# Performance work log

Measured on AMD Instinct MI355X. Metric: run time of the kernel, lower is better.

The kernel has to match this reference:

```python
import jax, jax.numpy as jnp
import numpy as np

B, C, O, H, W = 16, 256, 256, 64, 64
T_DIM, E, K = 512, 4, 3


def setup_inputs() -> dict:
    key = jax.random.key(0)
    ks = jax.random.split(key, 12)
    def rn(k, shape, s=0.02):
        return jax.random.normal(k, shape, jnp.float32) * s
    return dict(
        x=jax.random.normal(ks[0], (B, C, H, W), jnp.float32),
        time_emb=jax.random.normal(ks[1], (B, T_DIM), jnp.float32),
        Wq=rn(ks[2], (C, T_DIM)), bq=jnp.zeros((C,), jnp.float32),
        Wk=rn(ks[3], (C, C)), bk=jnp.zeros((C,), jnp.float32),
        Wv=rn(ks[4], (C, C)), bv=jnp.zeros((C,), jnp.float32),
        Wm1=rn(ks[5], (C // 4, C)), bm1=jnp.zeros((C // 4,), jnp.float32),
        Wm2=rn(ks[6], (C, C // 4)), bm2=jnp.zeros((C,), jnp.float32),
        Wc=rn(ks[7], (E, C)), bc=jnp.zeros((E,), jnp.float32),
        expert_w=rn(ks[8], (E, O, C, K, K), s=0.05),  # [E, O, C_in/groups, K, K]
        expert_b=rn(ks[9], (E, O), s=0.05),
    )


def reference(x, time_emb, Wq, bq, Wk, bk, Wv, bv, Wm1, bm1, Wm2, bm2, Wc, bc, expert_w, expert_b):
    # --- router (eval mode: no gating noise) ---
    pooled = x.mean(axis=(2, 3))                      # [B, C] == avg_pool over full HxW
    q = time_emb @ Wq.T + bq                          # [B, C]
    k = pooled @ Wk.T + bk                            # [B, C]
    attn = jax.nn.sigmoid(q * k)
    v = pooled @ Wv.T + bv
    x_att = v * attn
    h = jax.nn.gelu(x_att @ Wm1.T + bm1, approximate=False) @ Wm2.T + bm2
    x_mix = x_att + h
    logits = x_mix @ Wc.T + bc                        # [B, E]
    rw = jnp.tanh(logits)                             # routing weights [B, E]

    # --- per-sample expert-weight mixing ---
    w_eff = jnp.einsum('be,eoihw->boihw', rw, expert_w)  # [B, O, C, K, K]
    b_eff = rw @ expert_b                                 # [B, O]

    # --- per-sample conv (equivalent to groups=B trick) ---
    def conv_one(xb, wb):
        # xb: [C, H, W], wb: [O, C, K, K]
        return jax.lax.conv_general_dilated(
            xb[None], wb, window_strides=(1, 1), padding=[(1, 1), (1, 1)],
            dimension_numbers=('NCHW', 'OIHW', 'NCHW'))[0]

    out = jax.vmap(conv_one)(x, w_eff)                 # [B, O, H, W]
    return out + b_eff[:, :, None, None]
```

## Files before the change

kernel.cpp:

```cpp
#include <hip/hip_runtime.h>

typedef __bf16 bf16x8 __attribute__((ext_vector_type(8)));
typedef float f32x4 __attribute__((ext_vector_type(4)));

__device__ __forceinline__ unsigned short f2bf(float f) {
  union { float f; unsigned int u; } v;
  v.f = f;
  unsigned int r = v.u + 0x7FFFu + ((v.u >> 16) & 1u);
  return (unsigned short)(r >> 16);
}

__device__ __forceinline__ void load_lds16(const void* g, void* l) {
  __builtin_amdgcn_global_load_lds(
      (__attribute__((address_space(1))) void*)(void*)g,
      (__attribute__((address_space(3))) void*)l, 16, 0, 0);
}

__global__ void transpose_kernel(const float* __restrict__ x, unsigned short* __restrict__ xTpad,
                                 float* __restrict__ part) {
  int bid = blockIdx.x;
  int b = bid / 66, hp = bid % 66;
  unsigned short* rowbase = xTpad + ((size_t)(b * 66 + hp)) * 66 * 256;
  int t = threadIdx.x;
  if (hp == 0 || hp == 65) {
    uint4 z = make_uint4(0u, 0u, 0u, 0u);
    for (int i = t; i < 2112; i += 256) ((uint4*)rowbase)[i] = z;
    return;
  }
  int h = hp - 1;
  __shared__ unsigned short lds[64 * 264];
  __shared__ float psum[256];
  const float* xb = x + ((size_t)b * 256 * 64 + h) * 64;
  int lane = t & 63;
  int w0 = (t & 15) * 4;
  int sxw = ((t & 15) & 7) << 3;
  #pragma unroll
  for (int g = 0; g < 16; ++g) {
    int c = g * 16 + (t >> 4);
    int cx = c ^ sxw;
    float4 v = *(const float4*)&xb[(size_t)c * 4096 + w0];
    lds[(w0 + 0) * 264 + cx] = f2bf(v.x);
    lds[(w0 + 1) * 264 + cx] = f2bf(v.y);
    lds[(w0 + 2) * 264 + cx] = f2bf(v.z);
    lds[(w0 + 3) * 264 + cx] = f2bf(v.w);
    float s = v.x + v.y + v.z + v.w;
    s += __shfl_xor(s, 1); s += __shfl_xor(s, 2);
    s += __shfl_xor(s, 4); s += __shfl_xor(s, 8);
    if ((lane & 15) == 0) psum[c] = s;
  }
  __syncthreads();
  #pragma unroll
  for (int p = 0; p < 8; ++p) {
    int w = p * 8 + (t >> 5);
    int seg = t & 31;
    int sxr = ((w >> 2) & 7) << 3;
    uint4 u = *(const uint4*)&lds[w * 264 + ((seg * 8) ^ sxr)];
    *(uint4*)&rowbase[(w + 1) * 256 + seg * 8] = u;
  }
  if (t < 64) {
    uint4 z = make_uint4(0u, 0u, 0u, 0u);
    int row = (t >> 5) ? 65 : 0;
    *(uint4*)&rowbase[row * 256 + (t & 31) * 8] = z;
  }
  if (t < 256) part[((size_t)b * 64 + h) * 256 + t] = psum[t];
}

__global__ void router_kernel(
    const float* __restrict__ time_emb, const float* __restrict__ part,
    const float* __restrict__ Wq, const float* __restrict__ bq,
    const float* __restrict__ Wk, const float* __restrict__ bk,
    const float* __restrict__ Wv, const float* __restrict__ bv,
    const float* __restrict__ Wm1, const float* __restrict__ bm1,
    const float* __restrict__ Wm2, const float* __restrict__ bm2,
    const float* __restrict__ Wc, const float* __restrict__ bc,
    const float* __restrict__ expert_b,
    float* __restrict__ rw_out, float* __restrict__ beff_out) {
  int b = blockIdx.x, tid = threadIdx.x;
  int t = tid & 255;
  __shared__ float te[512], pl[256], qs[256], xa[256], m1s[64], xms[256], rws[4];
  te[tid] = time_emb[b * 512 + tid];
  if (tid < 256) {
    const float* pp = part + (size_t)b * 16384 + tid;
    float s0 = 0.f, s1 = 0.f, s2 = 0.f, s3 = 0.f,
          s4 = 0.f, s5 = 0.f, s6 = 0.f, s7 = 0.f;
    #pragma unroll
    for (int hh = 0; hh < 64; hh += 8) {
      s0 += pp[(hh + 0) * 256]; s1 += pp[(hh + 1) * 256];
      s2 += pp[(hh + 2) * 256]; s3 += pp[(hh + 3) * 256];
      s4 += pp[(hh + 4) * 256]; s5 += pp[(hh + 5) * 256];
      s6 += pp[(hh + 6) * 256]; s7 += pp[(hh + 7) * 256];
    }
    pl[tid] = (((s0 + s1) + (s2 + s3)) + ((s4 + s5) + (s6 + s7))) * (1.0f / 4096.0f);
  }
  __syncthreads();
  if (tid < 256) {
    float q = bq[t];
    const float4* wq4 = (const float4*)(Wq + (size_t)t * 512);
    #pragma unroll 4
    for (int i = 0; i < 128; ++i) {
      float4 w4 = wq4[i];
      q += w4.x * te[i*4] + w4.y * te[i*4+1] + w4.z * te[i*4+2] + w4.w * te[i*4+3];
    }
    qs[t] = q;
  } else {
    float k = bk[t], v = bv[t];
    const float4* wk4 = (const float4*)(Wk + (size_t)t * 256);
    const float4* wv4 = (const float4*)(Wv + (size_t)t * 256);
    #pragma unroll 4
    for (int i = 0; i < 64; ++i) {
      float4 a4 = wk4[i], b4 = wv4[i];
      float p0 = pl[i*4], p1 = pl[i*4+1], p2 = pl[i*4+2], p3 = pl[i*4+3];
      k += a4.x * p0 + a4.y * p1 + a4.z * p2 + a4.w * p3;
      v += b4.x * p0 + b4.y * p1 + b4.z * p2 + b4.w * p3;
    }
    xa[t] = k;
    xms[t] = v;
  }
  __syncthreads();
  if (tid < 256) {
    float k = xa[t], v = xms[t];
    float attn = 1.0f / (1.0f + expf(-(qs[t] * k)));
    qs[t] = v * attn;
  }
  __syncthreads();
  if (tid < 64) {
    float s = bm1[tid];
    const float4* w1 = (const float4*)(Wm1 + (size_t)tid * 256);
    #pragma unroll 4
    for (int i = 0; i < 64; ++i) {
      float4 w4 = w1[i];
      s += w4.x * qs[i*4] + w4.y * qs[i*4+1] + w4.z * qs[i*4+2] + w4.w * qs[i*4+3];
    }
    m1s[tid] = 0.5f * s * (1.0f + erff(s * 0.7071067811865476f));
  }
  __syncthreads();
  if (tid < 256) {
    float hsum = bm2[t];
    const float* w2 = Wm2 + (size_t)t * 64;
    for (int j = 0; j < 64; ++j) hsum += m1s[j] * w2[j];
    xms[t] = qs[t] + hsum;
  }
  __syncthreads();
  if (tid < 4) {
    float s = bc[tid];
    const float* wc = Wc + (size_t)tid * 256;
    for (int i = 0; i < 256; ++i) s += xms[i] * wc[i];
    float r = tanhf(s);
    rws[tid] = r;
    rw_out[b * 4 + tid] = r;
  }
  __syncthreads();
  if (tid < 256) {
    float be = 0.f;
    #pragma unroll
    for (int e = 0; e < 4; ++e) be += rws[e] * expert_b[e * 256 + t];
    beff_out[b * 256 + t] = be;
  }
}

__global__ void wmixT_kernel(const float* __restrict__ ew, const float* __restrict__ rw,
                             unsigned short* __restrict__ wmixT) {
  int b = blockIdx.x >> 4, ob = blockIdx.x & 15;
  int t = threadIdx.x;
  float r0 = rw[b * 4 + 0], r1 = rw[b * 4 + 1], r2 = rw[b * 4 + 2], r3 = rw[b * 4 + 3];
  unsigned short* dst = wmixT + (size_t)(b * 16 + ob) * 36864 + (t >> 3) * 128 + (t & 7);
  #pragma unroll 2
  for (int op = 0; op < 16; ++op) {
    int o = ob * 16 + op;
    const float* s0 = ew + ((size_t)(0 * 256 + o) * 256 + t) * 9;
    const float* s1 = ew + ((size_t)(1 * 256 + o) * 256 + t) * 9;
    const float* s2 = ew + ((size_t)(2 * 256 + o) * 256 + t) * 9;
    const float* s3 = ew + ((size_t)(3 * 256 + o) * 256 + t) * 9;
    #pragma unroll
    for (int tt = 0; tt < 9; ++tt) {
      float m = r0 * s0[tt] + r1 * s1[tt] + r2 * s2[tt] + r3 * s3[tt];
      dst[tt * 4096 + op * 8] = f2bf(m);
    }
  }
}

__global__ __launch_bounds__(512, 2) void conv_kernel(
    const unsigned short* __restrict__ xT, const unsigned short* __restrict__ wmixT,
    const float* __restrict__ beff, float* __restrict__ out) {
  __shared__ unsigned short Bs[2][16384];
  int bid = blockIdx.x;
  int b = ((bid & 7) << 1) | ((bid >> 7) & 1);
  int nt = (bid >> 3) & 15;
  int h0 = nt << 2;
  int tid = threadIdx.x;
  int wid = tid >> 6, lane = tid & 63;
  int lm = lane & 15, lg = lane >> 4;
  int wm = wid >> 1, wn = wid & 1;

  const unsigned short* xTb = xT + (size_t)b * 66 * 66 * 256;
  const unsigned short* wmA = wmixT + (size_t)(b * 16 + wm * 4) * 288 * 128 + lane * 8;

  int lr = lane >> 3;
  int slot_g = (lane & 7) ^ lr;
  int b_lane = lr * 256 + slot_g * 8;

  int sw0 = ((0 + lg) ^ (lm & 7)) * 8;
  int sw1 = ((4 + lg) ^ (lm & 7)) * 8;

  auto stB = [&](int buf, int kh, int cc, int kw, int q) {
    const unsigned short* src =
        xTb + (size_t)((h0 + q + kh) * 66 + wid * 8 + kw) * 256 + cc * 64 + b_lane;
    load_lds16(src, &Bs[buf][(q * 64 + wid * 8) * 64]);
  };

  f32x4 acc[4][8];
  #pragma unroll
  for (int mf = 0; mf < 4; ++mf)
    #pragma unroll
    for (int nf = 0; nf < 8; ++nf)
      acc[mf][nf] = (f32x4){0.f, 0.f, 0.f, 0.f};

  bf16x8 Ae[4][2], Ao[4][2];

  stB(0, 0, 0, 0, 0); stB(0, 0, 0, 0, 1); stB(0, 0, 0, 0, 2); stB(0, 0, 0, 0, 3);
  __builtin_amdgcn_sched_barrier(0);
  #pragma unroll
  for (int mf = 0; mf < 4; ++mf)
    #pragma unroll
    for (int kk = 0; kk < 2; ++kk)
      Ae[mf][kk] = *(const bf16x8*)(wmA + (size_t)(mf * 288 + kk * 4) * 128);
  asm volatile("s_waitcnt vmcnt(8)" ::: "memory");
  __builtin_amdgcn_s_barrier();

  auto tile_body = [&](int t, int buf, bf16x8 (&Acur)[4][2], bf16x8 (&Anext)[4][2])
      __attribute__((always_inline)) {
    bool st = (t < 35);
    if (st) {
      int tn = t + 1;
      int khn = tn / 12, rn = tn % 12, ccn = rn / 3, kwn = rn % 3;
      stB(buf ^ 1, khn, ccn, kwn, 0); stB(buf ^ 1, khn, ccn, kwn, 1);
      stB(buf ^ 1, khn, ccn, kwn, 2); stB(buf ^ 1, khn, ccn, kwn, 3);
      __builtin_amdgcn_sched_barrier(0);
      int kbase = (khn * 3 + kwn) * 32 + ccn * 8;
      #pragma unroll
      for (int mf = 0; mf < 4; ++mf)
        #pragma unroll
        for (int kk = 0; kk < 2; ++kk)
          Anext[mf][kk] = *(const bf16x8*)(wmA + (size_t)(mf * 288 + kbase + kk * 4) * 128);
    }
    #pragma unroll
    for (int nf = 0; nf < 8; ++nf) {
      bf16x8 b0 = *(const bf16x8*)&Bs[buf][(wn * 128 + nf * 16 + lm) * 64 + sw0];
      bf16x8 b1 = *(const bf16x8*)&Bs[buf][(wn * 128 + nf * 16 + lm) * 64 + sw1];
      #pragma unroll
      for (int mf = 0; mf < 4; ++mf) {
        acc[mf][nf] = __builtin_amdgcn_mfma_f32_16x16x32_bf16(Acur[mf][0], b0, acc[mf][nf], 0, 0, 0);
        acc[mf][nf] = __builtin_amdgcn_mfma_f32_16x16x32_bf16(Acur[mf][1], b1, acc[mf][nf], 0, 0, 0);
      }
    }
    if (st) {
      asm volatile("s_waitcnt vmcnt(8)" ::: "memory");
      __builtin_amdgcn_s_barrier();
    }
  };

  for (int i = 0; i < 18; ++i) {
    tile_body(2 * i, 0, Ae, Ao);
    tile_body(2 * i + 1, 1, Ao, Ae);
  }

  #pragma unroll
  for (int mf = 0; mf < 4; ++mf) {
    int o = wm * 64 + mf * 16 + lg * 4;
    float be0 = beff[b * 256 + o + 0];
    float be1 = beff[b * 256 + o + 1];
    float be2 = beff[b * 256 + o + 2];
    float be3 = beff[b * 256 + o + 3];
    #pragma unroll
    for (int nf = 0; nf < 8; ++nf) {
      int n = wn * 128 + nf * 16 + lm;
      int hh = h0 + (n >> 6), w = n & 63;
      float* op = out + (((size_t)(b * 256 + o)) * 64 + hh) * 64 + w;
      op[0]            = acc[mf][nf][0] + be0;
      op[4096]         = acc[mf][nf][1] + be1;
      op[2 * 4096]     = acc[mf][nf][2] + be2;
      op[3 * 4096]     = acc[mf][nf][3] + be3;
    }
  }
}

extern "C" void kernel_launch(void* const* d_in, const int* in_sizes, int n_in,
                              void* d_out, int out_size, void* d_ws, size_t ws_size,
                              hipStream_t stream) {
  const float* x        = (const float*)d_in[0];
  const float* time_emb = (const float*)d_in[1];
  const float* Wq = (const float*)d_in[2];
  const float* bq = (const float*)d_in[3];
  const float* Wk = (const float*)d_in[4];
  const float* bk = (const float*)d_in[5];
  const float* Wv = (const float*)d_in[6];
  const float* bv = (const float*)d_in[7];
  const float* Wm1 = (const float*)d_in[8];
  const float* bm1 = (const float*)d_in[9];
  const float* Wm2 = (const float*)d_in[10];
  const float* bm2 = (const float*)d_in[11];
  const float* Wc = (const float*)d_in[12];
  const float* bc = (const float*)d_in[13];
  const float* expert_w = (const float*)d_in[14];
  const float* expert_b = (const float*)d_in[15];
  float* out = (float*)d_out;

  char* ws = (char*)d_ws;
  float* rw   = (float*)(ws + 0);
  float* beff = (float*)(ws + 1024);
  float* part = (float*)(ws + 20480);
  unsigned short* xTpad = (unsigned short*)(ws + 1069056);
  unsigned short* wmixT = (unsigned short*)(ws + 1069056 + 35684352);

  transpose_kernel<<<1056, 256, 0, stream>>>(x, xTpad, part);
  router_kernel<<<16, 512, 0, stream>>>(time_emb, part, Wq, bq, Wk, bk, Wv, bv,
                                        Wm1, bm1, Wm2, bm2, Wc, bc, expert_b, rw, beff);
  wmixT_kernel<<<256, 256, 0, stream>>>(expert_w, rw, wmixT);
  conv_kernel<<<256, 512, 0, stream>>>(xTpad, wmixT, beff, out);
}
```

Measured before the change: 148.7 us.

## Read conv B operand directly from global and coalesce mixed-weight stores via LDS

The conv kernel stops staging the input patch tile into double-buffered LDS with global_load_lds and barriers. Each lane now loads its B fragments straight from global memory (relying on L1/L2 for reuse), which removes LDS traffic and the per-tile synchronisation. Separately, the weight-mixing kernel now stages its bf16 outputs in LDS and writes them as 16-byte vector stores instead of scattered 2-byte stores. The risk is higher global/L2 load pressure and exposed load latency in the conv main loop, since the B loads are no longer prefetched.

```diff
diff --git a/kernel.cpp b/kernel.cpp
--- a/kernel.cpp
+++ b/kernel.cpp
@@ -8,12 +8,6 @@
   v.f = f;
   unsigned int r = v.u + 0x7FFFu + ((v.u >> 16) & 1u);
   return (unsigned short)(r >> 16);
-}
-
-__device__ __forceinline__ void load_lds16(const void* g, void* l) {
-  __builtin_amdgcn_global_load_lds(
-      (__attribute__((address_space(1))) void*)(void*)g,
-      (__attribute__((address_space(3))) void*)l, 16, 0, 0);
 }
 
 __global__ void transpose_kernel(const float* __restrict__ x, unsigned short* __restrict__ xTpad,
@@ -162,9 +156,14 @@
                              unsigned short* __restrict__ wmixT) {
   int b = blockIdx.x >> 4, ob = blockIdx.x & 15;
   int t = threadIdx.x;
+  int wv = t >> 6, lane = t & 63;
+  __shared__ unsigned short rep[4][9 * 72];
+  unsigned short* myrep = rep[wv];
   float r0 = rw[b * 4 + 0], r1 = rw[b * 4 + 1], r2 = rw[b * 4 + 2], r3 = rw[b * 4 + 3];
-  unsigned short* dst = wmixT + (size_t)(b * 16 + ob) * 36864 + (t >> 3) * 128 + (t & 7);
-  #pragma unroll 2
+  unsigned short* dstb = wmixT + (size_t)(b * 16 + ob) * 36864;
+  int tt1 = lane >> 3, kcl1 = lane & 7;
+  int kcl2 = lane & 7;
+  #pragma unroll 1
   for (int op = 0; op < 16; ++op) {
     int o = ob * 16 + op;
     const float* s0 = ew + ((size_t)(0 * 256 + o) * 256 + t) * 9;
@@ -174,7 +173,15 @@
     #pragma unroll
     for (int tt = 0; tt < 9; ++tt) {
       float m = r0 * s0[tt] + r1 * s1[tt] + r2 * s2[tt] + r3 * s3[tt];
-      dst[tt * 4096 + op * 8] = f2bf(m);
+      myrep[tt * 72 + lane] = f2bf(m);
+    }
+    {
+      uint4 v1 = *(const uint4*)&myrep[tt1 * 72 + kcl1 * 8];
+      *(uint4*)&dstb[((tt1 * 32 + wv * 8 + kcl1) * 128) + op * 8] = v1;
+      if (lane < 8) {
+        uint4 v2 = *(const uint4*)&myrep[8 * 72 + kcl2 * 8];
+        *(uint4*)&dstb[((8 * 32 + wv * 8 + kcl2) * 128) + op * 8] = v2;
+      }
     }
   }
 }
@@ -182,7 +189,6 @@
 __global__ __launch_bounds__(512, 2) void conv_kernel(
     const unsigned short* __restrict__ xT, const unsigned short* __restrict__ wmixT,
     const float* __restrict__ beff, float* __restrict__ out) {
-  __shared__ unsigned short Bs[2][16384];
   int bid = blockIdx.x;
   int b = ((bid & 7) << 1) | ((bid >> 7) & 1);
   int nt = (bid >> 3) & 15;
@@ -193,20 +199,14 @@
   int wm = wid >> 1, wn = wid & 1;
 
   const unsigned short* xTb = xT + (size_t)b * 66 * 66 * 256;
-  const unsigned short* wmA = wmixT + (size_t)(b * 16 + wm * 4) * 288 * 128 + lane * 8;
-
-  int lr = lane >> 3;
-  int slot_g = (lane & 7) ^ lr;
-  int b_lane = lr * 256 + slot_g * 8;
-
-  int sw0 = ((0 + lg) ^ (lm & 7)) * 8;
-  int sw1 = ((4 + lg) ^ (lm & 7)) * 8;
-
-  auto stB = [&](int buf, int kh, int cc, int kw, int q) {
-    const unsigned short* src =
-        xTb + (size_t)((h0 + q + kh) * 66 + wid * 8 + kw) * 256 + cc * 64 + b_lane;
-    load_lds16(src, &Bs[buf][(q * 64 + wid * 8) * 64]);
-  };
+  const unsigned short* wmA = wmixT + (size_t)(b * 16 + wm * 4) * 36864 + lane * 8;
+
+  const unsigned short* bbase[8];
+  #pragma unroll
+  for (int nf = 0; nf < 8; ++nf) {
+    int n = wn * 128 + nf * 16 + lm;
+    bbase[nf] = xTb + (size_t)((h0 + (n >> 6)) * 66 + (n & 63)) * 256 + lg * 8;
+  }
 
   f32x4 acc[4][8];
   #pragma unroll
@@ -216,26 +216,19 @@
       acc[mf][nf] = (f32x4){0.f, 0.f, 0.f, 0.f};
 
   bf16x8 Ae[4][2], Ao[4][2];
-
-  stB(0, 0, 0, 0, 0); stB(0, 0, 0, 0, 1); stB(0, 0, 0, 0, 2); stB(0, 0, 0, 0, 3);
-  __builtin_amdgcn_sched_barrier(0);
   #pragma unroll
   for (int mf = 0; mf < 4; ++mf)
     #pragma unroll
     for (int kk = 0; kk < 2; ++kk)
       Ae[mf][kk] = *(const bf16x8*)(wmA + (size_t)(mf * 288 + kk * 4) * 128);
-  asm volatile("s_waitcnt vmcnt(8)" ::: "memory");
-  __builtin_amdgcn_s_barrier();
-
-  auto tile_body = [&](int t, int buf, bf16x8 (&Acur)[4][2], bf16x8 (&Anext)[4][2])
+
+  auto tile_body = [&](int t, bf16x8 (&Acur)[4][2], bf16x8 (&Anext)[4][2])
       __attribute__((always_inline)) {
-    bool st = (t < 35);
-    if (st) {
+    int kh = t / 12, r = t % 12, cc = r / 3, kw = r % 3;
+    int boff = (kh * 66 + kw) * 256 + cc * 64;
+    if (t < 35) {
       int tn = t + 1;
       int khn = tn / 12, rn = tn % 12, ccn = rn / 3, kwn = rn % 3;
-      stB(buf ^ 1, khn, ccn, kwn, 0); stB(buf ^ 1, khn, ccn, kwn, 1);
-      stB(buf ^ 1, khn, ccn, kwn, 2); stB(buf ^ 1, khn, ccn, kwn, 3);
-      __builtin_amdgcn_sched_barrier(0);
       int kbase = (khn * 3 + kwn) * 32 + ccn * 8;
       #pragma unroll
       for (int mf = 0; mf < 4; ++mf)
@@ -245,23 +238,19 @@
     }
     #pragma unroll
     for (int nf = 0; nf < 8; ++nf) {
-      bf16x8 b0 = *(const bf16x8*)&Bs[buf][(wn * 128 + nf * 16 + lm) * 64 + sw0];
-      bf16x8 b1 = *(const bf16x8*)&Bs[buf][(wn * 128 + nf * 16 + lm) * 64 + sw1];
+      bf16x8 b0 = *(const bf16x8*)(bbase[nf] + boff);
+      bf16x8 b1 = *(const bf16x8*)(bbase[nf] + boff + 32);
       #pragma unroll
       for (int mf = 0; mf < 4; ++mf) {
         acc[mf][nf] = __builtin_amdgcn_mfma_f32_16x16x32_bf16(Acur[mf][0], b0, acc[mf][nf], 0, 0, 0);
         acc[mf][nf] = __builtin_amdgcn_mfma_f32_16x16x32_bf16(Acur[mf][1], b1, acc[mf][nf], 0, 0, 0);
       }
     }
-    if (st) {
-      asm volatile("s_waitcnt vmcnt(8)" ::: "memory");
-      __builtin_amdgcn_s_barrier();
-    }
   };
 
   for (int i = 0; i < 18; ++i) {
-    tile_body(2 * i, 0, Ae, Ao);
-    tile_body(2 * i + 1, 1, Ao, Ae);
+    tile_body(2 * i, Ae, Ao);
+    tile_body(2 * i + 1, Ao, Ae);
   }
 
   #pragma unroll
```

Result: slower. 231.6 us (+55.7%).
